# Kernel tuning notes

Hardware: AMD Instinct MI355X
Metric: run time of the kernel (lower is better)

## Reference

```python
import jax, jax.numpy as jnp
import numpy as np

B, T, H = 262144, 15, 64


def setup_inputs() -> dict:
    key = jax.random.key(0)
    ks = jax.random.split(key, 8)
    s_ih = 1.0 / np.sqrt(H)
    return {
        "x": jax.random.normal(ks[0], (B, T), dtype=jnp.float32),
        # PyTorch GRU params: W_ih [3H, input_size=1], W_hh [3H, H], biases [3H]
        "W_ih": jax.random.uniform(ks[1], (3 * H, 1), jnp.float32, -s_ih, s_ih),
        "W_hh": jax.random.uniform(ks[2], (3 * H, H), jnp.float32, -s_ih, s_ih),
        "b_ih": jax.random.uniform(ks[3], (3 * H,), jnp.float32, -s_ih, s_ih),
        "b_hh": jax.random.uniform(ks[4], (3 * H,), jnp.float32, -s_ih, s_ih),
        "W_fc": jax.random.uniform(ks[5], (2, H), jnp.float32, -s_ih, s_ih),
        "b_fc": jax.random.uniform(ks[6], (2,), jnp.float32, -s_ih, s_ih),
    }


def reference(x, W_ih, W_hh, b_ih, b_hh, W_fc, b_fc):
    # x: [B, T]; each scalar feature is one timestep of a 1-dim GRU input.
    w_in = W_ih[:, 0]  # [3H] since input_size == 1

    def step(h, x_t):
        # x_t: [B]; input gates are just outer product with w_in (input_size=1)
        xg = x_t[:, None] * w_in[None, :] + b_ih          # [B, 3H]
        hg = h @ W_hh.T + b_hh                            # [B, 3H]
        r = jax.nn.sigmoid(xg[:, :H] + hg[:, :H])
        z = jax.nn.sigmoid(xg[:, H:2 * H] + hg[:, H:2 * H])
        n = jnp.tanh(xg[:, 2 * H:] + r * hg[:, 2 * H:])
        h_new = (1.0 - z) * n + z * h
        return h_new, None

    h0 = jnp.zeros((x.shape[0], H), dtype=x.dtype)
    h_last, _ = jax.lax.scan(step, h0, x.T)  # scan over time dim
    logits = h_last @ W_fc.T + b_fc          # [B, 2]
    return logits
```

## Files before the change

kernel.cpp:

```cpp
#include <hip/hip_runtime.h>

#define T_STEPS 15
#define ROWS_PER_BLOCK 128
#define B_TOTAL 262144
#define LOG2E 1.4426950408889634f

typedef _Float16 half8 __attribute__((ext_vector_type(8)));
typedef _Float16 half4 __attribute__((ext_vector_type(4)));
typedef __fp16   fp16x2 __attribute__((ext_vector_type(2)));
typedef float f32x4 __attribute__((ext_vector_type(4)));

#define MFMA_INIT(acc, a, b, cz) \
    asm("v_mfma_f32_16x16x32_f16 %0, %1, %2, %3" : "=&v"(acc) : "v"(a), "v"(b), "v"(cz))
#define MFMA_ACC(acc, a, b) \
    asm("v_mfma_f32_16x16x32_f16 %0, %1, %2, %0" : "+v"(acc) : "v"(a), "v"(b))

__device__ __forceinline__ int swz(int row, int e) {
    return (row * 64 + e) ^ ((row & 7) << 3);
}

__global__ __launch_bounds__(256, 2) void gru_mfma_kernel(
    const float* __restrict__ x,
    const float* __restrict__ W_ih,
    const float* __restrict__ W_hh,
    const float* __restrict__ b_ih,
    const float* __restrict__ b_hh,
    const float* __restrict__ W_fc,
    const float* __restrict__ b_fc,
    float* __restrict__ out)
{
    __shared__ _Float16 wlds[192 * 64];
    __shared__ float    xlds[T_STEPS * ROWS_PER_BLOCK];
    __shared__ _Float16 hst[8][16 * 64];

    const int tid  = threadIdx.x;
    const int wave = tid >> 6;
    const int lane = tid & 63;
    const int c    = lane & 15;
    const int g4   = lane >> 4;
    const int r0   = blockIdx.x * ROWS_PER_BLOCK;

    for (int idx = tid; idx < 192 * 64; idx += 256) {
        int n = idx >> 6, s = idx & 63;
        int korig = (s & 3) * 16 + (s >> 2);
        float scale = (n < 128) ? LOG2E : (2.0f * LOG2E);
        wlds[swz(n, s)] = (_Float16)(W_hh[n * 64 + korig] * scale);
    }
    for (int idx = tid; idx < ROWS_PER_BLOCK * T_STEPS; idx += 256) {
        int row = idx / T_STEPS, t = idx - row * T_STEPS;
        xlds[t * ROWS_PER_BLOCK + row] = x[r0 * T_STEPS + idx];
    }
    __syncthreads();

    float wihr[4], wihz[4], wihn[4], sr[4], sz[4], seedn[4], bihn[4];
#pragma unroll
    for (int tq = 0; tq < 4; ++tq) {
        int jn = tq * 16 + c;
        wihr[tq]  = W_ih[jn] * LOG2E;
        wihz[tq]  = W_ih[64 + jn] * LOG2E;
        wihn[tq]  = W_ih[128 + jn] * (2.0f * LOG2E);
        sr[tq]    = (b_ih[jn] + b_hh[jn]) * LOG2E;
        sz[tq]    = (b_ih[64 + jn] + b_hh[64 + jn]) * LOG2E;
        seedn[tq] = b_hh[128 + jn] * (2.0f * LOG2E);
        bihn[tq]  = b_ih[128 + jn] * (2.0f * LOG2E);
    }

    const int eS0 = c * 64 + (((g4 * 8) + 0)  ^ ((c & 7) << 3));
    const int eS1 = c * 64 + (((g4 * 8) + 32) ^ ((c & 7) << 3));
    const int bytesS0 = eS0 * 2;
    const int bytesS1 = eS1 * 2;
    const _Float16* aA0 = &hst[wave * 2 + 0][eS0];
    const _Float16* aA1 = &hst[wave * 2 + 0][eS1];
    const _Float16* aB0 = &hst[wave * 2 + 1][eS0];
    const _Float16* aB1 = &hst[wave * 2 + 1][eS1];
    _Float16* wr[2][4];
#pragma unroll
    for (int s = 0; s < 2; ++s)
#pragma unroll
        for (int reg = 0; reg < 4; ++reg) {
            int row = g4 * 4 + reg;
            wr[s][reg] = &hst[wave * 2 + s][row * 64 + ((c * 4) ^ ((row & 7) << 3))];
        }

    const f32x4 zero4 = (f32x4){0.0f, 0.0f, 0.0f, 0.0f};

    f32x4 accr[2][4], accz[2][4], accn[2][4];
#pragma unroll
    for (int s = 0; s < 2; ++s)
#pragma unroll
        for (int tq = 0; tq < 4; ++tq) {
            accr[s][tq] = zero4;
            accz[s][tq] = zero4;
            accn[s][tq] = zero4;
        }

    float h[2][4][4];
#pragma unroll
    for (int s = 0; s < 2; ++s)
#pragma unroll
        for (int tq = 0; tq < 4; ++tq)
#pragma unroll
            for (int reg = 0; reg < 4; ++reg) h[s][tq][reg] = 0.0f;

    const char* wbase = (const char*)&wlds[0];

#pragma unroll 1
    for (int t = 0; t < T_STEPS; ++t) {
        if (t > 0) {
            int ofA = bytesS0, ofB = bytesS1;
            asm volatile("" : "+v"(ofA), "+v"(ofB));
            const char* bp0 = wbase + ofA;
            const char* bp1 = wbase + ofB;

            half8 A0sA = *(const half8*)aA0;
            half8 A1sA = *(const half8*)aA1;
            half8 A0sB = *(const half8*)aB0;
            half8 A1sB = *(const half8*)aB1;
#pragma unroll
            for (int tq = 0; tq < 4; ++tq) {
                half8 Br0 = *(const half8*)(bp0 + tq * 2048);
                half8 Br1 = *(const half8*)(bp1 + tq * 2048);
                half8 Bz0 = *(const half8*)(bp0 + (4 + tq) * 2048);
                half8 Bz1 = *(const half8*)(bp1 + (4 + tq) * 2048);
                half8 Bn0 = *(const half8*)(bp0 + (8 + tq) * 2048);
                half8 Bn1 = *(const half8*)(bp1 + (8 + tq) * 2048);
                MFMA_INIT(accr[0][tq], A0sA, Br0, zero4);
                MFMA_ACC (accr[0][tq], A1sA, Br1);
                MFMA_INIT(accz[0][tq], A0sA, Bz0, zero4);
                MFMA_ACC (accz[0][tq], A1sA, Bz1);
                MFMA_INIT(accn[0][tq], A0sA, Bn0, zero4);
                MFMA_ACC (accn[0][tq], A1sA, Bn1);
                MFMA_INIT(accr[1][tq], A0sB, Br0, zero4);
                MFMA_ACC (accr[1][tq], A1sB, Br1);
                MFMA_INIT(accz[1][tq], A0sB, Bz0, zero4);
                MFMA_ACC (accz[1][tq], A1sB, Bz1);
                MFMA_INIT(accn[1][tq], A0sB, Bn0, zero4);
                MFMA_ACC (accn[1][tq], A1sB, Bn1);
                if (tq < 3) __builtin_amdgcn_sched_barrier(0);
            }
            __builtin_amdgcn_sched_barrier(0);
            asm volatile("s_nop 7\n\ts_nop 7");
            __builtin_amdgcn_sched_barrier(0);
        }

#pragma unroll
        for (int s = 0; s < 2; ++s) {
            f32x4 xt4 = *(const f32x4*)&xlds[t * ROWS_PER_BLOCK + wave * 32 + s * 16 + g4 * 4];
#pragma unroll
            for (int reg = 0; reg < 4; ++reg) {
                float xt = xt4[reg];
                float hnv[4];
#pragma unroll
                for (int tq = 0; tq < 4; ++tq) {
                    float pr = accr[s][tq][reg] + __builtin_fmaf(xt, wihr[tq], sr[tq]);
                    float er = __builtin_amdgcn_exp2f(-pr);
                    float rg = __builtin_amdgcn_rcpf(1.0f + er);
                    float pz = accz[s][tq][reg] + __builtin_fmaf(xt, wihz[tq], sz[tq]);
                    float ez = __builtin_amdgcn_exp2f(-pz);
                    float na = __builtin_fmaf(rg, accn[s][tq][reg],
                                __builtin_fmaf(rg, seedn[tq],
                                 __builtin_fmaf(xt, wihn[tq], bihn[tq])));
                    float en = __builtin_amdgcn_exp2f(-na);
                    float A  = 1.0f + en;
                    float Cc = 1.0f + ez;
                    float D  = A * Cc;
                    float R  = __builtin_amdgcn_rcpf(D);
                    float P  = __builtin_fmaf(-en, ez, ez);
                    float num = __builtin_fmaf(h[s][tq][reg], A, P);
                    float hn = num * R;
                    h[s][tq][reg] = hn;
                    hnv[tq] = hn;
                }
                fp16x2 h01 = __builtin_amdgcn_cvt_pkrtz(hnv[0], hnv[1]);
                fp16x2 h23 = __builtin_amdgcn_cvt_pkrtz(hnv[2], hnv[3]);
                half4 vh;
                vh[0] = (_Float16)h01[0]; vh[1] = (_Float16)h01[1];
                vh[2] = (_Float16)h23[0]; vh[3] = (_Float16)h23[1];
                *(half4*)wr[s][reg] = vh;
            }
        }
    }

    const float* wfc = W_fc;
    const float* bfc = b_fc;
    asm volatile("" : "+v"(wfc), "+v"(bfc));
    float wfc0[4], wfc1[4];
#pragma unroll
    for (int tq = 0; tq < 4; ++tq) {
        wfc0[tq] = wfc[tq * 16 + c];
        wfc1[tq] = wfc[64 + tq * 16 + c];
    }
#pragma unroll
    for (int s = 0; s < 2; ++s)
#pragma unroll
    for (int reg = 0; reg < 4; ++reg) {
        float s0 = 0.0f, s1 = 0.0f;
#pragma unroll
        for (int tq = 0; tq < 4; ++tq) {
            s0 = __builtin_fmaf(h[s][tq][reg], wfc0[tq], s0);
            s1 = __builtin_fmaf(h[s][tq][reg], wfc1[tq], s1);
        }
#pragma unroll
        for (int m = 1; m < 16; m <<= 1) {
            s0 += __shfl_xor(s0, m, 64);
            s1 += __shfl_xor(s1, m, 64);
        }
        if (c == 0) {
            int gr = r0 + wave * 32 + s * 16 + g4 * 4 + reg;
            out[gr * 2 + 0] = s0 + bfc[0];
            out[gr * 2 + 1] = s1 + bfc[1];
        }
    }
}

extern "C" void kernel_launch(void* const* d_in, const int* in_sizes, int n_in,
                              void* d_out, int out_size, void* d_ws, size_t ws_size,
                              hipStream_t stream) {
    const float* x    = (const float*)d_in[0];
    const float* W_ih = (const float*)d_in[1];
    const float* W_hh = (const float*)d_in[2];
    const float* b_ih = (const float*)d_in[3];
    const float* b_hh = (const float*)d_in[4];
    const float* W_fc = (const float*)d_in[5];
    const float* b_fc = (const float*)d_in[6];
    float* out = (float*)d_out;

    dim3 grid(B_TOTAL / ROWS_PER_BLOCK);
    dim3 block(256);
    gru_mfma_kernel<<<grid, block, 0, stream>>>(x, W_ih, W_hh, b_ih, b_hh, W_fc, b_fc, out);
}
```

Measured before the change: 215.9 us.

## Software-pipeline GRU steps by interleaving MFMA of one subtile with gates of other

Measured after the change: 208.5 us. -3.4%, faster.

```diff
diff --git a/kernel.cpp b/kernel.cpp
--- a/kernel.cpp
+++ b/kernel.cpp
@@ -18,6 +18,71 @@
 __device__ __forceinline__ int swz(int row, int e) {
     return (row * 64 + e) ^ ((row & 7) << 3);
 }
+
+#define MFMA_BLOCK(S, AP0, AP1)  do { \
+    int ofA = bytesS0, ofB = bytesS1; \
+    asm volatile("" : "+v"(ofA), "+v"(ofB)); \
+    const char* bp0 = wbase + ofA; \
+    const char* bp1 = wbase + ofB; \
+    half8 A0 = *(const half8*)(AP0); \
+    half8 A1 = *(const half8*)(AP1); \
+    _Pragma("unroll") \
+    for (int tq = 0; tq < 4; ++tq) { \
+        half8 Br0 = *(const half8*)(bp0 + tq * 2048); \
+        half8 Br1 = *(const half8*)(bp1 + tq * 2048); \
+        half8 Bz0 = *(const half8*)(bp0 + (4 + tq) * 2048); \
+        half8 Bz1 = *(const half8*)(bp1 + (4 + tq) * 2048); \
+        half8 Bn0 = *(const half8*)(bp0 + (8 + tq) * 2048); \
+        half8 Bn1 = *(const half8*)(bp1 + (8 + tq) * 2048); \
+        MFMA_INIT(accr[S][tq], A0, Br0, zero4); \
+        MFMA_ACC (accr[S][tq], A1, Br1); \
+        MFMA_INIT(accz[S][tq], A0, Bz0, zero4); \
+        MFMA_ACC (accz[S][tq], A1, Bz1); \
+        MFMA_INIT(accn[S][tq], A0, Bn0, zero4); \
+        MFMA_ACC (accn[S][tq], A1, Bn1); \
+        if (tq < 3) __builtin_amdgcn_sched_barrier(0); \
+    } \
+} while (0)
+
+#define HAZPAD() do { \
+    __builtin_amdgcn_sched_barrier(0); \
+    asm volatile("s_nop 7"); \
+    __builtin_amdgcn_sched_barrier(0); \
+} while (0)
+
+#define GATES(S, TT) do { \
+    f32x4 xt4 = *(const f32x4*)&xlds[(TT) * ROWS_PER_BLOCK + wave * 32 + (S) * 16 + g4 * 4]; \
+    _Pragma("unroll") \
+    for (int reg = 0; reg < 4; ++reg) { \
+        float xt = xt4[reg]; \
+        float hnv[4]; \
+        _Pragma("unroll") \
+        for (int tq = 0; tq < 4; ++tq) { \
+            float pr = accr[S][tq][reg] + __builtin_fmaf(xt, wihr[tq], sr[tq]); \
+            float er = __builtin_amdgcn_exp2f(-pr); \
+            float rg = __builtin_amdgcn_rcpf(1.0f + er); \
+            float pz = accz[S][tq][reg] + __builtin_fmaf(xt, wihz[tq], sz[tq]); \
+            float ez = __builtin_amdgcn_exp2f(-pz); \
+            float na = __builtin_fmaf(rg, accn[S][tq][reg], \
+                        __builtin_fmaf(rg, seedn[tq], \
+                         __builtin_fmaf(xt, wihn[tq], bihn[tq]))); \
+            float en = __builtin_amdgcn_exp2f(-na); \
+            float A_ = 1.0f + en; \
+            float C_ = 1.0f + ez; \
+            float R_ = __builtin_amdgcn_rcpf(A_ * C_); \
+            float P_ = __builtin_fmaf(-en, ez, ez); \
+            float hn = __builtin_fmaf(h[S][tq][reg], A_, P_) * R_; \
+            h[S][tq][reg] = hn; \
+            hnv[tq] = hn; \
+        } \
+        fp16x2 h01 = __builtin_amdgcn_cvt_pkrtz(hnv[0], hnv[1]); \
+        fp16x2 h23 = __builtin_amdgcn_cvt_pkrtz(hnv[2], hnv[3]); \
+        half4 vh; \
+        vh[0] = (_Float16)h01[0]; vh[1] = (_Float16)h01[1]; \
+        vh[2] = (_Float16)h23[0]; vh[3] = (_Float16)h23[1]; \
+        *(half4*)wr[S][reg] = vh; \
+    } \
+} while (0)
 
 __global__ __launch_bounds__(256, 2) void gru_mfma_kernel(
     const float* __restrict__ x,
@@ -104,82 +169,23 @@
 
     const char* wbase = (const char*)&wlds[0];
 
+    GATES(0, 0);
+    MFMA_BLOCK(0, aA0, aA1);
+    GATES(1, 0);
+
 #pragma unroll 1
-    for (int t = 0; t < T_STEPS; ++t) {
-        if (t > 0) {
-            int ofA = bytesS0, ofB = bytesS1;
-            asm volatile("" : "+v"(ofA), "+v"(ofB));
-            const char* bp0 = wbase + ofA;
-            const char* bp1 = wbase + ofB;
-
-            half8 A0sA = *(const half8*)aA0;
-            half8 A1sA = *(const half8*)aA1;
-            half8 A0sB = *(const half8*)aB0;
-            half8 A1sB = *(const half8*)aB1;
-#pragma unroll
-            for (int tq = 0; tq < 4; ++tq) {
-                half8 Br0 = *(const half8*)(bp0 + tq * 2048);
-                half8 Br1 = *(const half8*)(bp1 + tq * 2048);
-                half8 Bz0 = *(const half8*)(bp0 + (4 + tq) * 2048);
-                half8 Bz1 = *(const half8*)(bp1 + (4 + tq) * 2048);
-                half8 Bn0 = *(const half8*)(bp0 + (8 + tq) * 2048);
-                half8 Bn1 = *(const half8*)(bp1 + (8 + tq) * 2048);
-                MFMA_INIT(accr[0][tq], A0sA, Br0, zero4);
-                MFMA_ACC (accr[0][tq], A1sA, Br1);
-                MFMA_INIT(accz[0][tq], A0sA, Bz0, zero4);
-                MFMA_ACC (accz[0][tq], A1sA, Bz1);
-                MFMA_INIT(accn[0][tq], A0sA, Bn0, zero4);
-                MFMA_ACC (accn[0][tq], A1sA, Bn1);
-                MFMA_INIT(accr[1][tq], A0sB, Br0, zero4);
-                MFMA_ACC (accr[1][tq], A1sB, Br1);
-                MFMA_INIT(accz[1][tq], A0sB, Bz0, zero4);
-                MFMA_ACC (accz[1][tq], A1sB, Bz1);
-                MFMA_INIT(accn[1][tq], A0sB, Bn0, zero4);
-                MFMA_ACC (accn[1][tq], A1sB, Bn1);
-                if (tq < 3) __builtin_amdgcn_sched_barrier(0);
-            }
-            __builtin_amdgcn_sched_barrier(0);
-            asm volatile("s_nop 7\n\ts_nop 7");
-            __builtin_amdgcn_sched_barrier(0);
-        }
-
-#pragma unroll
-        for (int s = 0; s < 2; ++s) {
-            f32x4 xt4 = *(const f32x4*)&xlds[t * ROWS_PER_BLOCK + wave * 32 + s * 16 + g4 * 4];
-#pragma unroll
-            for (int reg = 0; reg < 4; ++reg) {
-                float xt = xt4[reg];
-                float hnv[4];
-#pragma unroll
-                for (int tq = 0; tq < 4; ++tq) {
-                    float pr = accr[s][tq][reg] + __builtin_fmaf(xt, wihr[tq], sr[tq]);
-                    float er = __builtin_amdgcn_exp2f(-pr);
-                    float rg = __builtin_amdgcn_rcpf(1.0f + er);
-                    float pz = accz[s][tq][reg] + __builtin_fmaf(xt, wihz[tq], sz[tq]);
-                    float ez = __builtin_amdgcn_exp2f(-pz);
-                    float na = __builtin_fmaf(rg, accn[s][tq][reg],
-                                __builtin_fmaf(rg, seedn[tq],
-                                 __builtin_fmaf(xt, wihn[tq], bihn[tq])));
-                    float en = __builtin_amdgcn_exp2f(-na);
-                    float A  = 1.0f + en;
-                    float Cc = 1.0f + ez;
-                    float D  = A * Cc;
-                    float R  = __builtin_amdgcn_rcpf(D);
-                    float P  = __builtin_fmaf(-en, ez, ez);
-                    float num = __builtin_fmaf(h[s][tq][reg], A, P);
-                    float hn = num * R;
-                    h[s][tq][reg] = hn;
-                    hnv[tq] = hn;
-                }
-                fp16x2 h01 = __builtin_amdgcn_cvt_pkrtz(hnv[0], hnv[1]);
-                fp16x2 h23 = __builtin_amdgcn_cvt_pkrtz(hnv[2], hnv[3]);
-                half4 vh;
-                vh[0] = (_Float16)h01[0]; vh[1] = (_Float16)h01[1];
-                vh[2] = (_Float16)h23[0]; vh[3] = (_Float16)h23[1];
-                *(half4*)wr[s][reg] = vh;
-            }
-        }
-    }
+    for (int t = 1; t < T_STEPS - 1; ++t) {
+        MFMA_BLOCK(1, aB0, aB1);
+        HAZPAD();
+        GATES(0, t);
+        MFMA_BLOCK(0, aA0, aA1);
+        HAZPAD();
+        GATES(1, t);
+    }
+    MFMA_BLOCK(1, aB0, aB1);
+    HAZPAD();
+    GATES(0, T_STEPS - 1);
+    GATES(1, T_STEPS - 1);
 
     const float* wfc = W_fc;
     const float* bfc = b_fc;
```
